# Kernel optimization log

Hardware: AMD Instinct MI355X
Metric: run time of the kernel (lower is better)

The kernel has to match this reference:

```python
import jax, jax.numpy as jnp
import numpy as np

D = 256; H = 8; HD = D // H; NK = 32; NLAYERS = 4; FF = 4 * D
B = 8; M = 768; N = 128; LT = 64; T = M + N + LT
SCALE = 1.0 / float(np.sqrt(HD))


def layer_norm(x, s, b):
    mu = x.mean(-1, keepdims=True)
    var = ((x - mu) ** 2).mean(-1, keepdims=True)
    return (x - mu) * jax.lax.rsqrt(var + 1e-5) * s + b


def sine_embed(pos, d):
    # MTR gen_sineembed_for_position: half dims for y, half for x, interleaved sin/cos
    half = d // 2
    dim_t = jnp.power(10000.0, 2.0 * (jnp.arange(half) // 2).astype(jnp.float32) / half)
    scale = 2.0 * np.pi
    def inter(e):
        return jnp.stack([jnp.sin(e[:, 0::2]), jnp.cos(e[:, 1::2])], -1).reshape(e.shape[0], -1)
    ex = pos[:, 0:1] * scale / dim_t
    ey = pos[:, 1:2] * scale / dim_t
    return jnp.concatenate([inter(ey), inter(ex)], -1)


def setup_inputs() -> dict:
    key = jax.random.key(0)
    ks = jax.random.split(key, 24)
    s = 0.02
    inp = {
        'map_token': jax.random.normal(ks[0], (B, M, D), jnp.float32),
        'agent_token': jax.random.normal(ks[1], (B, N, D), jnp.float32),
        'light_token': jax.random.normal(ks[2], (B, LT, D), jnp.float32),
        'map_position': jax.random.uniform(ks[3], (B, M, 2), jnp.float32) * 100.0,
        'agent_position': jax.random.uniform(ks[4], (B, N, 2), jnp.float32) * 100.0,
        'light_position': jax.random.uniform(ks[5], (B, LT, 2), jnp.float32) * 100.0,
        'map_valid_mask': jnp.ones((B, M), bool),
        'agent_valid_mask': jnp.ones((B, N), bool),
        'light_valid_mask': jnp.ones((B, LT), bool),
        'Wq': jax.random.normal(ks[6], (NLAYERS, D, D), jnp.float32) * s,
        'bq': jnp.zeros((NLAYERS, D), jnp.float32),
        'Wk': jax.random.normal(ks[7], (NLAYERS, D, D), jnp.float32) * s,
        'bk': jnp.zeros((NLAYERS, D), jnp.float32),
        'Wv': jax.random.normal(ks[8], (NLAYERS, D, D), jnp.float32) * s,
        'bv': jnp.zeros((NLAYERS, D), jnp.float32),
        'Wo': jax.random.normal(ks[9], (NLAYERS, D, D), jnp.float32) * s,
        'bo': jnp.zeros((NLAYERS, D), jnp.float32),
        'W1': jax.random.normal(ks[10], (NLAYERS, D, FF), jnp.float32) * s,
        'b1': jnp.zeros((NLAYERS, FF), jnp.float32),
        'W2': jax.random.normal(ks[11], (NLAYERS, FF, D), jnp.float32) * s,
        'b2': jnp.zeros((NLAYERS, D), jnp.float32),
        'ln1_s': jnp.ones((NLAYERS, D), jnp.float32),
        'ln1_b': jnp.zeros((NLAYERS, D), jnp.float32),
        'ln2_s': jnp.ones((NLAYERS, D), jnp.float32),
        'ln2_b': jnp.zeros((NLAYERS, D), jnp.float32),
    }
    return inp


def reference(map_token, agent_token, light_token, map_position, agent_position, light_position,
              map_valid_mask, agent_valid_mask, light_valid_mask,
              Wq, bq, Wk, bk, Wv, bv, Wo, bo, W1, b1, W2, b2, ln1_s, ln1_b, ln2_s, ln2_b):
    x = jnp.concatenate([map_token, agent_token, light_token], 1)             # [B,T,D]
    pos = jnp.concatenate([map_position, agent_position, light_position], 1)[..., :2]  # [B,T,2]
    # all tokens valid -> masked compaction is a static reshape
    xs = x.reshape(B * T, D)
    ps = pos.reshape(B * T, 2)
    # KNN within each scene (includes self, like knn_batch_mlogk on same set)
    d2 = jnp.sum((pos[:, :, None, :] - pos[:, None, :, :]) ** 2, -1)          # [B,T,T]
    _, idx = jax.lax.top_k(-d2, NK)                                            # [B,T,NK] local indices
    idx = (idx + (jnp.arange(B) * T)[:, None, None]).reshape(B * T, NK)        # global flat indices
    pe = sine_embed(ps, D)                                                     # [B*T,D]
    out = xs
    for l in range(NLAYERS):
        qk = out + pe
        q = (qk @ Wq[l] + bq[l]).reshape(-1, H, HD)
        k = (qk @ Wk[l] + bk[l]).reshape(-1, H, HD)
        v = (out @ Wv[l] + bv[l]).reshape(-1, H, HD)
        kn = k[idx]                                                            # [BT,NK,H,HD] gather
        vn = v[idx]
        att = jax.nn.softmax(jnp.einsum('nhd,nkhd->nhk', q, kn) * SCALE, axis=-1)
        a = jnp.einsum('nhk,nkhd->nhd', att, vn).reshape(-1, D) @ Wo[l] + bo[l]
        out = layer_norm(out + a, ln1_s[l], ln1_b[l])
        ff = jax.nn.relu(out @ W1[l] + b1[l]) @ W2[l] + b2[l]
        out = layer_norm(out + ff, ln2_s[l], ln2_b[l])
    full = out.reshape(B, T, D)
    return full[:, :M], full[:, M:M + N], full[:, M + N:]
```

## Files before the change

### kernel.cpp

```cpp
#include <hip/hip_runtime.h>
#include <math.h>

#define BB 8
#define MTOK 768
#define NTOK 128
#define LTOK 64
#define TT 960
#define BT 7680
#define DD 256
#define HH 8
#define HD 32
#define KNN 32
#define FFD 1024
#define NLAYERS 4
#define SCALE_ATT 0.17677669529663687f

typedef __attribute__((ext_vector_type(8))) short bfrag_t;
typedef __attribute__((ext_vector_type(4))) float accfrag_t;

__device__ __forceinline__ float b2f(unsigned short u) {
  union { unsigned int i; float f; } c; c.i = ((unsigned int)u) << 16; return c.f;
}
__device__ __forceinline__ unsigned short f2b(float f) {
  union { float f; unsigned int i; } c; c.f = f;
  return (unsigned short)((c.i + 0x7fffu + ((c.i >> 16) & 1u)) >> 16);
}
__device__ __forceinline__ float load_elem(const void* p, size_t i, int f) {
  return f ? b2f(((const unsigned short*)p)[i]) : ((const float*)p)[i];
}
__device__ __forceinline__ size_t pk_addr(int row, int col, int nks) {
  return ((size_t)((row >> 4) * nks + (col >> 5)) << 9)
       + (size_t)(((((col >> 3) & 3) << 4) + (row & 15)) * 8 + (col & 7));
}
__device__ __forceinline__ uint4 pack8(const float* v) {
  uint4 u;
  u.x = (unsigned)f2b(v[0]) | ((unsigned)f2b(v[1]) << 16);
  u.y = (unsigned)f2b(v[2]) | ((unsigned)f2b(v[3]) << 16);
  u.z = (unsigned)f2b(v[4]) | ((unsigned)f2b(v[5]) << 16);
  u.w = (unsigned)f2b(v[6]) | ((unsigned)f2b(v[7]) << 16);
  return u;
}
__device__ __forceinline__ int swiz_tok(int blk) { return (blk & 7) * TT + (blk >> 3); }

__global__ __launch_bounds__(256)
void detect_kernel(const void* tok, int* flag) {
  __shared__ int cnt;
  if (threadIdx.x == 0) cnt = 0;
  __syncthreads();
  const unsigned short* u = (const unsigned short*)tok;
  int ok = 0;
  for (int i = threadIdx.x; i < 1024; i += 256) {
    int e = (u[i] >> 7) & 0xFF;
    if (e >= 100 && e <= 140) ok++;
  }
  atomicAdd(&cnt, ok);
  __syncthreads();
  if (threadIdx.x == 0) *flag = (cnt >= 922) ? 1 : 0;
}

#define FB_BQ 0
#define FB_BK 1024
#define FB_BV 2048
#define FB_BO 3072
#define FB_B1 4096
#define FB_B2 8192
#define FB_LN1S 9216
#define FB_LN1B 10240
#define FB_LN2S 11264
#define FB_LN2B 12288
#define FB_TOTAL 13312
struct ParamSrc { const void* p[13]; };
__global__ __launch_bounds__(256)
void conv_misc_kernel(ParamSrc ps, const int* flag, float* __restrict__ dst,
                      float* __restrict__ posf) {
  int f = *flag;
  if (blockIdx.x < BB) {
    int b = blockIdx.x;
    for (int t = threadIdx.x; t < TT * 2; t += 256) {
      int tok = t >> 1, c = t & 1;
      const void* p; size_t idx;
      if (tok < MTOK)             { p = ps.p[10]; idx = (size_t)(b * MTOK + tok) * 2 + c; }
      else if (tok < MTOK + NTOK) { p = ps.p[11]; idx = (size_t)(b * NTOK + tok - MTOK) * 2 + c; }
      else                        { p = ps.p[12]; idx = (size_t)(b * LTOK + tok - MTOK - NTOK) * 2 + c; }
      posf[((size_t)b * TT + tok) * 2 + c] = load_elem(p, idx, f);
    }
    return;
  }
  int i = (blockIdx.x - BB) * 256 + threadIdx.x;
  if (i >= FB_TOTAL) return;
  int src; size_t off;
  if (i < 4096)      { src = i >> 10;              off = i & 1023; }
  else if (i < 8192) { src = 4;                    off = i - 4096; }
  else               { src = 5 + ((i - 8192) >> 10); off = (i - 8192) & 1023; }
  dst[i] = load_elem(ps.p[src], off, f);
}

struct PackSrc { const void* s[6]; };
__global__ __launch_bounds__(256)
void packW_kernel(PackSrc w, const int* flag,
                  unsigned short* __restrict__ Wqkvpk, unsigned short* __restrict__ Wopk,
                  unsigned short* __restrict__ W1pk, unsigned short* __restrict__ W2pk) {
  int f = *flag;
  int id = blockIdx.x * 256 + threadIdx.x;
  const void* src; unsigned short* dst; int layer, e, K, N;
  if (id < 786432) {
    layer = id / 196608; int rest = id % 196608; int sel = rest / 65536; e = rest % 65536;
    src = w.s[sel]; dst = Wqkvpk + id; K = 256; N = 256;
  } else if (id < 1048576) {
    int off = id - 786432; layer = off / 65536; e = off % 65536;
    src = w.s[3]; dst = Wopk + off; K = 256; N = 256;
  } else if (id < 2097152) {
    int off = id - 1048576; layer = off / 262144; e = off % 262144;
    src = w.s[4]; dst = W1pk + off; K = 256; N = 1024;
  } else {
    int off = id - 2097152; layer = off / 262144; e = off % 262144;
    src = w.s[5]; dst = W2pk + off; K = 1024; N = 256;
  }
  int nks = K >> 5;
  int cb = e / (nks * 512);
  int ks = (e / 512) % nks;
  int lane = (e >> 3) & 63, j = e & 7;
  int col = cb * 16 + (lane & 15);
  int k = ks * 32 + (lane >> 4) * 8 + j;
  size_t si = (size_t)layer * K * N + (size_t)k * N + col;
  *dst = f ? ((const unsigned short*)src)[si] : f2b(((const float*)src)[si]);
}

__global__ __launch_bounds__(256)
void prep_kernel(const void* mt, const void* at, const void* lt,
                 const float* __restrict__ posf, const int* flag,
                 unsigned short* __restrict__ pe_b, float* __restrict__ out_f,
                 unsigned short* __restrict__ pk1, unsigned short* __restrict__ qkpk) {
  int n = swiz_tok(blockIdx.x), d = threadIdx.x;
  int b = n / TT, t = n - b * TT;
  int f = *flag;
  const void* src; size_t si;
  if (t < MTOK)              { src = mt; si = (size_t)(b * MTOK + t) * DD + d; }
  else if (t < MTOK + NTOK)  { src = at; si = (size_t)(b * NTOK + (t - MTOK)) * DD + d; }
  else                       { src = lt; si = (size_t)(b * LTOK + (t - MTOK - NTOK)) * DD + d; }
  float x = load_elem(src, si, f);
  float px = posf[((size_t)b * TT + t) * 2 + 0];
  float py = posf[((size_t)b * TT + t) * 2 + 1];
  float coord = (d < 128) ? py : px;
  int j = d & 127;
  float expo = (float)(2 * (j >> 1)) / 128.0f;
  float dim_t = powf(10000.0f, expo);
  float e = coord * 6.283185307179586f / dim_t;
  float p = (j & 1) ? cosf(e) : sinf(e);
  size_t o = (size_t)n * DD + d;
  pe_b[o] = f2b(p);
  out_f[o] = x;
  size_t pa = pk_addr(n, d, 8);
  pk1[pa] = f2b(x);
  qkpk[pa] = f2b(x + p);
}

__device__ __forceinline__ unsigned long long shfl_xor_u64(unsigned long long v, int m) {
  unsigned lo = (unsigned)v, hi = (unsigned)(v >> 32);
  lo = (unsigned)__shfl_xor((int)lo, m);
  hi = (unsigned)__shfl_xor((int)hi, m);
  return ((unsigned long long)hi << 32) | (unsigned long long)lo;
}
__device__ __forceinline__ unsigned long long shfl_u64(unsigned long long v, int srcLane) {
  unsigned lo = (unsigned)v, hi = (unsigned)(v >> 32);
  lo = (unsigned)__shfl((int)lo, srcLane);
  hi = (unsigned)__shfl((int)hi, srcLane);
  return ((unsigned long long)hi << 32) | (unsigned long long)lo;
}
__device__ __forceinline__ unsigned long long bitonic64(unsigned long long key, int lane) {
#pragma unroll
  for (int kk = 2; kk <= 64; kk <<= 1) {
#pragma unroll
    for (int j = kk >> 1; j > 0; j >>= 1) {
      unsigned long long other = shfl_xor_u64(key, j);
      bool small_ = (lane & j) == 0;
      bool dir = (lane & kk) == 0;
      bool keep = ((key < other) == (small_ == dir));
      key = keep ? key : other;
    }
  }
  return key;
}

__global__ __launch_bounds__(256)
void knn_kernel(const float* __restrict__ posf, int* __restrict__ idx_out) {
  __shared__ float sx[TT], sy[TT];
  __shared__ unsigned long long cbuf[4][64];
  int b = blockIdx.x & 7;
  int qbase = (blockIdx.x >> 3) * 4;
  for (int t = threadIdx.x; t < TT; t += 256) {
    sx[t] = posf[((size_t)b * TT + t) * 2 + 0];
    sy[t] = posf[((size_t)b * TT + t) * 2 + 1];
  }
  __syncthreads();
  int wave = threadIdx.x >> 6, lane = threadIdx.x & 63;
  int t = qbase + wave;
  float qx = sx[t], qy = sy[t];

  unsigned long long k[15];
#pragma unroll
  for (int c = 0; c < 15; c++) {
    int j = c * 64 + lane;
    float dx = qx - sx[j], dy = qy - sy[j];
    float d2 = __fadd_rn(__fmul_rn(dx, dx), __fmul_rn(dy, dy));
    k[c] = ((unsigned long long)__float_as_uint(d2) << 32) | (unsigned)j;
  }

  unsigned long long lm = k[0];
#pragma unroll
  for (int c = 1; c < 15; c++) lm = (k[c] < lm) ? k[c] : lm;

  unsigned long long sm = bitonic64(lm, lane);
  unsigned long long thr = shfl_u64(sm, 31);

  int c_l = 0;
#pragma unroll
  for (int c = 0; c < 15; c++) c_l += (k[c] <= thr) ? 1 : 0;
  int inc = c_l;
#pragma unroll
  for (int o = 1; o < 64; o <<= 1) {
    int tt = __shfl_up(inc, o);
    inc += (lane >= o) ? tt : 0;
  }
  int total = __shfl(inc, 63);
  int pos = inc - c_l;

  if (total <= 64) {
    unsigned long long* wb = cbuf[wave];
#pragma unroll
    for (int c = 0; c < 15; c++) {
      if (k[c] <= thr) { wb[pos] = k[c]; pos++; }
    }
    unsigned long long cand = (lane < total) ? wb[lane] : ~0ull;
    cand = bitonic64(cand, lane);
    if (lane < KNN)
      idx_out[((size_t)(b * TT + t)) * KNN + lane] = b * TT + (int)(cand & 0xFFFFFFFFu);
  } else {
    unsigned res = 0;
    for (int i = 0; i < KNN; i++) {
      unsigned long long m = k[0];
#pragma unroll
      for (int c = 1; c < 15; c++) m = (k[c] < m) ? k[c] : m;
#pragma unroll
      for (int o = 32; o > 0; o >>= 1) {
        unsigned long long om = shfl_xor_u64(m, o);
        m = (om < m) ? om : m;
      }
      if (lane == i) res = (unsigned)(m & 0xFFFFFFFFu);
      int owner = (int)(m & 63u), ch = (int)(((unsigned)(m & 0xFFFFFFFFu)) >> 6);
      if (lane == owner) {
#pragma unroll
        for (int c = 0; c < 15; c++) if (c == ch) k[c] = ~0ull;
      }
    }
    if (lane < KNN)
      idx_out[((size_t)(b * TT + t)) * KNN + lane] = b * TT + (int)res;
  }
}

template<int NKS>
__device__ __forceinline__ void wavegemm(const unsigned short* __restrict__ Apk,
                                         const unsigned short* __restrict__ Bpk,
                                         int rb, int cb0, accfrag_t (&acc)[4]) {
  const int lane = threadIdx.x & 63;
  accfrag_t z = {0.f, 0.f, 0.f, 0.f};
#pragma unroll
  for (int nt = 0; nt < 4; nt++) acc[nt] = z;
  const unsigned short* ap = Apk + ((size_t)rb * NKS * 512 + lane * 8);
  const unsigned short* bp = Bpk + ((size_t)cb0 * NKS * 512 + lane * 8);
#pragma unroll 4
  for (int ks = 0; ks < NKS; ks++) {
    bfrag_t a = *(const bfrag_t*)(ap + ks * 512);
#pragma unroll
    for (int nt = 0; nt < 4; nt++) {
      bfrag_t b = *(const bfrag_t*)(bp + (size_t)(nt * NKS + ks) * 512);
      acc[nt] = __builtin_amdgcn_mfma_f32_16x16x32_bf16(a, b, acc[nt], 0, 0, 0);
    }
  }
}

__global__ __launch_bounds__(256)
void qkv_kernel(const unsigned short* __restrict__ qkpk,
                const unsigned short* __restrict__ outpk,
                const unsigned short* __restrict__ Wl,
                const float* __restrict__ pb, int l,
                unsigned short* __restrict__ QKV) {
  int scene = blockIdx.x & 7, r = blockIdx.x >> 3;
  int rbg = r % 15, cgall = r / 15;
  int wave = threadIdx.x >> 6, lane = threadIdx.x & 63;
  int rb = scene * 60 + rbg * 4 + wave;
  int sel = cgall >> 2, cg = cgall & 3;
  const unsigned short* A = (sel < 2) ? qkpk : outpk;
  const unsigned short* B = Wl + sel * 65536;
  const float* bias = pb + sel * 1024 + l * 256;
  accfrag_t acc[4];
  wavegemm<8>(A, B, rb, cg * 4, acc);
  int l16 = lane & 15, lq = lane >> 4;
  unsigned short* C = QKV + (size_t)sel * BT * DD;
#pragma unroll
  for (int nt = 0; nt < 4; nt++) {
    int col = cg * 64 + nt * 16 + l16;
    float bv = bias[col];
#pragma unroll
    for (int r4 = 0; r4 < 4; r4++) {
      int row = rb * 16 + lq * 4 + r4;
      C[(size_t)row * DD + col] = f2b(acc[nt][r4] + bv);
    }
  }
}

__global__ __launch_bounds__(256)
void attn_kernel(const unsigned short* __restrict__ QKV,
                 const int* __restrict__ idx,
                 unsigned short* __restrict__ attnpk) {
  __shared__ unsigned short kn[KNN][DD + 8];
  __shared__ unsigned short vn[KNN][DD + 8];
  __shared__ float qs[DD];
  __shared__ float att[HH][KNN];
  __shared__ int nb[KNN];
  const unsigned short* Q = QKV;
  const unsigned short* K = QKV + (size_t)BT * DD;
  const unsigned short* V = QKV + 2 * (size_t)BT * DD;
  int n = swiz_tok(blockIdx.x), tid = threadIdx.x;
  if (tid < KNN) nb[tid] = idx[n * KNN + tid];
  qs[tid] = b2f(Q[(size_t)n * DD + tid]);
  __syncthreads();
#pragma unroll
  for (int p = 0; p < 4; p++) {
    int e = p * 256 + tid;
    int r = e >> 5, c8 = (e & 31) * 8;
    int srow = nb[r];
    *(uint4*)(&kn[r][c8]) = *(const uint4*)(K + (size_t)srow * DD + c8);
    *(uint4*)(&vn[r][c8]) = *(const uint4*)(V + (size_t)srow * DD + c8);
  }
  __syncthreads();
  int h = tid >> 5, kk = tid & 31;
  float dot = 0.0f;
#pragma unroll
  for (int d = 0; d < HD; d++) dot += qs[h * HD + d] * b2f(kn[kk][h * HD + d]);
  float sc = dot * SCALE_ATT;
  float mx = sc;
#pragma unroll
  for (int o = 16; o > 0; o >>= 1) mx = fmaxf(mx, __shfl_xor(mx, o, 32));
  float ex = expf(sc - mx);
  float sm = ex;
#pragma unroll
  for (int o = 16; o > 0; o >>= 1) sm += __shfl_xor(sm, o, 32);
  att[h][kk] = ex / sm;
  __syncthreads();
  int d = kk;
  float oacc = 0.0f;
#pragma unroll
  for (int k2 = 0; k2 < KNN; k2++) oacc += att[h][k2] * b2f(vn[k2][h * HD + d]);
  attnpk[pk_addr(n, tid, 8)] = f2b(oacc);
}

__global__ __launch_bounds__(256)
void wo_ln1_kernel(const unsigned short* __restrict__ attnpk,
                   const unsigned short* __restrict__ Wl,
                   const float* __restrict__ bo,
                   float* __restrict__ yf,
                   unsigned short* __restrict__ xpk,
                   const float* __restrict__ g, const float* __restrict__ bta) {
  __shared__ float ps1[4][16], ps2[4][16];
  int scene = blockIdx.x & 7, rbs = blockIdx.x >> 3;
  int wave = threadIdx.x >> 6, lane = threadIdx.x & 63;
  int rb = scene * 60 + rbs;
  accfrag_t acc[4];
  wavegemm<8>(attnpk, Wl, rb, wave * 4, acc);
  int l16 = lane & 15, lq = lane >> 4;
  float val[4][4];
  float s[4] = {0.f, 0.f, 0.f, 0.f}, s2[4] = {0.f, 0.f, 0.f, 0.f};
#pragma unroll
  for (int nt = 0; nt < 4; nt++) {
    int col = wave * 64 + nt * 16 + l16;
    float bv = bo[col];
#pragma unroll
    for (int r4 = 0; r4 < 4; r4++) {
      int row = rb * 16 + lq * 4 + r4;
      float x = acc[nt][r4] + bv + yf[(size_t)row * DD + col];
      val[nt][r4] = x; s[r4] += x; s2[r4] += x * x;
    }
  }
#pragma unroll
  for (int o = 1; o < 16; o <<= 1) {
#pragma unroll
    for (int r4 = 0; r4 < 4; r4++) { s[r4] += __shfl_xor(s[r4], o); s2[r4] += __shfl_xor(s2[r4], o); }
  }
  if (l16 == 0) {
#pragma unroll
    for (int r4 = 0; r4 < 4; r4++) { ps1[wave][lq * 4 + r4] = s[r4]; ps2[wave][lq * 4 + r4] = s2[r4]; }
  }
  __syncthreads();
  float mu[4], rstd[4];
#pragma unroll
  for (int r4 = 0; r4 < 4; r4++) {
    int r16 = lq * 4 + r4;
    float ts  = ps1[0][r16] + ps1[1][r16] + ps1[2][r16] + ps1[3][r16];
    float ts2 = ps2[0][r16] + ps2[1][r16] + ps2[2][r16] + ps2[3][r16];
    mu[r4] = ts * (1.0f / 256.0f);
    float var = ts2 * (1.0f / 256.0f) - mu[r4] * mu[r4];
    rstd[r4] = 1.0f / sqrtf(fmaxf(var, 0.f) + 1e-5f);
  }
#pragma unroll
  for (int nt = 0; nt < 4; nt++) {
    int col = wave * 64 + nt * 16 + l16;
    float gg = g[col], bb = bta[col];
#pragma unroll
    for (int r4 = 0; r4 < 4; r4++) {
      int row = rb * 16 + lq * 4 + r4;
      float y = (val[nt][r4] - mu[r4]) * rstd[r4] * gg + bb;
      yf[(size_t)row * DD + col] = y;
      xpk[pk_addr(row, col, 8)] = f2b(y);
    }
  }
}

__global__ __launch_bounds__(256)
void ffn1_kernel(const unsigned short* __restrict__ xpk,
                 const unsigned short* __restrict__ Wl,
                 const float* __restrict__ b1,
                 unsigned short* __restrict__ hpk) {
  int scene = blockIdx.x & 7, r = blockIdx.x >> 3;
  int rbg = r % 15, cg = r / 15;
  int wave = threadIdx.x >> 6, lane = threadIdx.x & 63;
  int rb = scene * 60 + rbg * 4 + wave;
  accfrag_t acc[4];
  wavegemm<8>(xpk, Wl, rb, cg * 4, acc);
  int l16 = lane & 15, lq = lane >> 4;
#pragma unroll
  for (int nt = 0; nt < 4; nt++) {
    int col = cg * 64 + nt * 16 + l16;
    float bv = b1[col];
#pragma unroll
    for (int r4 = 0; r4 < 4; r4++) {
      int row = rb * 16 + lq * 4 + r4;
      hpk[pk_addr(row, col, 32)] = f2b(fmaxf(acc[nt][r4] + bv, 0.0f));
    }
  }
}

template<bool LAST>
__global__ __launch_bounds__(256)
void ffn2_ln2_kernel(const unsigned short* __restrict__ hpk,
                     const unsigned short* __restrict__ Wl,
                     const float* __restrict__ b2,
                     float* __restrict__ yf,
                     unsigned short* __restrict__ outpk, unsigned short* __restrict__ qkpk,
                     const unsigned short* __restrict__ pe_b,
                     const float* __restrict__ g, const float* __restrict__ bta,
                     void* __restrict__ dout, const int* __restrict__ flag) {
  __shared__ float ps1[4][16], ps2[4][16];
  int scene = blockIdx.x & 7, rbs = blockIdx.x >> 3;
  int wave = threadIdx.x >> 6, lane = threadIdx.x & 63;
  int rb = scene * 60 + rbs;
  accfrag_t acc[4];
  wavegemm<32>(hpk, Wl, rb, wave * 4, acc);
  int l16 = lane & 15, lq = lane >> 4;
  float val[4][4];
  float s[4] = {0.f, 0.f, 0.f, 0.f}, s2[4] = {0.f, 0.f, 0.f, 0.f};
#pragma unroll
  for (int nt = 0; nt < 4; nt++) {
    int col = wave * 64 + nt * 16 + l16;
    float bv = b2[col];
#pragma unroll
    for (int r4 = 0; r4 < 4; r4++) {
      int row = rb * 16 + lq * 4 + r4;
      float x = acc[nt][r4] + bv + yf[(size_t)row * DD + col];
      val[nt][r4] = x; s[r4] += x; s2[r4] += x * x;
    }
  }
#pragma unroll
  for (int o = 1; o < 16; o <<= 1) {
#pragma unroll
    for (int r4 = 0; r4 < 4; r4++) { s[r4] += __shfl_xor(s[r4], o); s2[r4] += __shfl_xor(s2[r4], o); }
  }
  if (l16 == 0) {
#pragma unroll
    for (int r4 = 0; r4 < 4; r4++) { ps1[wave][lq * 4 + r4] = s[r4]; ps2[wave][lq * 4 + r4] = s2[r4]; }
  }
  __syncthreads();
  float mu[4], rstd[4];
#pragma unroll
  for (int r4 = 0; r4 < 4; r4++) {
    int r16 = lq * 4 + r4;
    float ts  = ps1[0][r16] + ps1[1][r16] + ps1[2][r16] + ps1[3][r16];
    float ts2 = ps2[0][r16] + ps2[1][r16] + ps2[2][r16] + ps2[3][r16];
    mu[r4] = ts * (1.0f / 256.0f);
    float var = ts2 * (1.0f / 256.0f) - mu[r4] * mu[r4];
    rstd[r4] = 1.0f / sqrtf(fmaxf(var, 0.f) + 1e-5f);
  }
  int fl = LAST ? *flag : 0;
#pragma unroll
  for (int nt = 0; nt < 4; nt++) {
    int col = wave * 64 + nt * 16 + l16;
    float gg = g[col], bb = bta[col];
#pragma unroll
    for (int r4 = 0; r4 < 4; r4++) {
      int row = rb * 16 + lq * 4 + r4;
      float y = (val[nt][r4] - mu[r4]) * rstd[r4] * gg + bb;
      if (!LAST) {
        yf[(size_t)row * DD + col] = y;
        outpk[pk_addr(row, col, 8)] = f2b(y);
        float q = y + b2f(pe_b[(size_t)row * DD + col]);
        qkpk[pk_addr(row, col, 8)] = f2b(q);
      } else {
        int t = rbs * 16 + lq * 4 + r4;
        size_t o;
        if (t < MTOK)             o = (size_t)(scene * MTOK + t) * DD + col;
        else if (t < MTOK + NTOK) o = (size_t)BB * MTOK * DD + (size_t)(scene * NTOK + (t - MTOK)) * DD + col;
        else                      o = (size_t)BB * MTOK * DD + (size_t)BB * NTOK * DD
                                    + (size_t)(scene * LTOK + (t - MTOK - NTOK)) * DD + col;
        if (fl) ((unsigned short*)dout)[o] = f2b(y);
        else    ((float*)dout)[o] = y;
      }
    }
  }
}

extern "C" void kernel_launch(void* const* d_in, const int* in_sizes, int n_in,
                              void* d_out, int out_size, void* d_ws, size_t ws_size,
                              hipStream_t stream) {
  const void* map_tok   = d_in[0];
  const void* agent_tok = d_in[1];
  const void* light_tok = d_in[2];
  const void* map_pos   = d_in[3];
  const void* agent_pos = d_in[4];
  const void* light_pos = d_in[5];
  const void* Wq  = d_in[9];
  const void* bq  = d_in[10];
  const void* Wk  = d_in[11];
  const void* bk  = d_in[12];
  const void* Wv  = d_in[13];
  const void* bv  = d_in[14];
  const void* Wo  = d_in[15];
  const void* bo  = d_in[16];
  const void* W1  = d_in[17];
  const void* b1  = d_in[18];
  const void* W2  = d_in[19];
  const void* b2  = d_in[20];
  const void* ln1s = d_in[21];
  const void* ln1b = d_in[22];
  const void* ln2s = d_in[23];
  const void* ln2b = d_in[24];

  size_t off = 0;
  char* base = (char*)d_ws;
  auto take = [&](size_t bytes) { char* p = base + off; off += (bytes + 255) & ~(size_t)255; return (void*)p; };
  int*   flag  = (int*)take(256);
  float* posf  = (float*)take((size_t)BT * 2 * 4);
  float* pbuf  = (float*)take((size_t)FB_TOTAL * 4);
  unsigned short* pe_b = (unsigned short*)take((size_t)BT * DD * 2);
  float* out_f = (float*)take((size_t)BT * DD * 4);
  unsigned short* pk1  = (unsigned short*)take((size_t)BT * DD * 2);
  unsigned short* qkpk = (unsigned short*)take((size_t)BT * DD * 2);
  unsigned short* QKV  = (unsigned short*)take((size_t)3 * BT * DD * 2);
  unsigned short* attnpk = (unsigned short*)take((size_t)BT * DD * 2);
  unsigned short* hpk  = (unsigned short*)take((size_t)BT * FFD * 2);
  int* idxb = (int*)take((size_t)BT * KNN * 4);
  unsigned short* Wqkvpk = (unsigned short*)take((size_t)NLAYERS * 3 * DD * DD * 2);
  unsigned short* Wopk   = (unsigned short*)take((size_t)NLAYERS * DD * DD * 2);
  unsigned short* W1pk   = (unsigned short*)take((size_t)NLAYERS * DD * FFD * 2);
  unsigned short* W2pk   = (unsigned short*)take((size_t)NLAYERS * DD * FFD * 2);

  detect_kernel<<<1, 256, 0, stream>>>(map_tok, flag);
  ParamSrc ps; ps.p[0]=bq; ps.p[1]=bk; ps.p[2]=bv; ps.p[3]=bo; ps.p[4]=b1;
  ps.p[5]=b2; ps.p[6]=ln1s; ps.p[7]=ln1b; ps.p[8]=ln2s; ps.p[9]=ln2b;
  ps.p[10]=map_pos; ps.p[11]=agent_pos; ps.p[12]=light_pos;
  conv_misc_kernel<<<BB + (FB_TOTAL + 255) / 256, 256, 0, stream>>>(ps, flag, pbuf, posf);

  PackSrc pw; pw.s[0]=Wq; pw.s[1]=Wk; pw.s[2]=Wv; pw.s[3]=Wo; pw.s[4]=W1; pw.s[5]=W2;
  packW_kernel<<<12288, 256, 0, stream>>>(pw, flag, Wqkvpk, Wopk, W1pk, W2pk);

  prep_kernel<<<BT, 256, 0, stream>>>(map_tok, agent_tok, light_tok, posf, flag,
                                      pe_b, out_f, pk1, qkpk);
  knn_kernel<<<1920, 256, 0, stream>>>(posf, idxb);

  for (int l = 0; l < NLAYERS; l++) {
    qkv_kernel<<<1440, 256, 0, stream>>>(qkpk, pk1, Wqkvpk + (size_t)l * 3 * 65536,
                                         pbuf, l, QKV);
    attn_kernel<<<BT, 256, 0, stream>>>(QKV, idxb, attnpk);
    wo_ln1_kernel<<<480, 256, 0, stream>>>(attnpk, Wopk + (size_t)l * 65536,
                                           pbuf + FB_BO + l * 256, out_f, pk1,
                                           pbuf + FB_LN1S + l * 256, pbuf + FB_LN1B + l * 256);
    ffn1_kernel<<<1920, 256, 0, stream>>>(pk1, W1pk + (size_t)l * 262144,
                                          pbuf + FB_B1 + l * 1024, hpk);
    if (l < NLAYERS - 1)
      ffn2_ln2_kernel<false><<<480, 256, 0, stream>>>(hpk, W2pk + (size_t)l * 262144,
                                                      pbuf + FB_B2 + l * 256, out_f, pk1, qkpk, pe_b,
                                                      pbuf + FB_LN2S + l * 256, pbuf + FB_LN2B + l * 256,
                                                      d_out, flag);
    else
      ffn2_ln2_kernel<true><<<480, 256, 0, stream>>>(hpk, W2pk + (size_t)l * 262144,
                                                     pbuf + FB_B2 + l * 256, out_f, pk1, qkpk, pe_b,
                                                     pbuf + FB_LN2S + l * 256, pbuf + FB_LN2B + l * 256,
                                                     d_out, flag);
  }
}
```

Baseline: 473.2 us.

## Fuse Wo+LN1, FFN1 and FFN2+LN2 into a single per-row-block kernel

Merges the three post-attention kernels into one kernel per 16-row block. The LN1 output and the ReLU hidden activations stay in shared memory instead of going through the global hpk buffer, and the residual is kept in registers. This removes two launches per layer and the global round-trip of the 1024-wide hidden tensor. In exchange, FFN1 drops from 1920 blocks to 480, each block uses about 40KB of LDS which limits occupancy, and every block rereads the full W1 and W2 matrices.

```diff
diff --git a/kernel.cpp b/kernel.cpp
--- a/kernel.cpp
+++ b/kernel.cpp
@@ -31,14 +31,6 @@
 __device__ __forceinline__ size_t pk_addr(int row, int col, int nks) {
   return ((size_t)((row >> 4) * nks + (col >> 5)) << 9)
        + (size_t)(((((col >> 3) & 3) << 4) + (row & 15)) * 8 + (col & 7));
-}
-__device__ __forceinline__ uint4 pack8(const float* v) {
-  uint4 u;
-  u.x = (unsigned)f2b(v[0]) | ((unsigned)f2b(v[1]) << 16);
-  u.y = (unsigned)f2b(v[2]) | ((unsigned)f2b(v[3]) << 16);
-  u.z = (unsigned)f2b(v[4]) | ((unsigned)f2b(v[5]) << 16);
-  u.w = (unsigned)f2b(v[6]) | ((unsigned)f2b(v[7]) << 16);
-  return u;
 }
 __device__ __forceinline__ int swiz_tok(int blk) { return (blk & 7) * TT + (blk >> 3); }
 
@@ -205,7 +197,6 @@
     float d2 = __fadd_rn(__fmul_rn(dx, dx), __fmul_rn(dy, dy));
     k[c] = ((unsigned long long)__float_as_uint(d2) << 32) | (unsigned)j;
   }
-
   unsigned long long lm = k[0];
 #pragma unroll
   for (int c = 1; c < 15; c++) lm = (k[c] < lm) ? k[c] : lm;
@@ -355,21 +346,32 @@
   attnpk[pk_addr(n, tid, 8)] = f2b(oacc);
 }
 
-__global__ __launch_bounds__(256)
-void wo_ln1_kernel(const unsigned short* __restrict__ attnpk,
-                   const unsigned short* __restrict__ Wl,
-                   const float* __restrict__ bo,
-                   float* __restrict__ yf,
-                   unsigned short* __restrict__ xpk,
-                   const float* __restrict__ g, const float* __restrict__ bta) {
+template<bool LAST>
+__global__ __launch_bounds__(256)
+void ffn_block_kernel(const unsigned short* __restrict__ attnpk,
+                      const unsigned short* __restrict__ Wo,
+                      const unsigned short* __restrict__ W1,
+                      const unsigned short* __restrict__ W2,
+                      const float* __restrict__ bo,
+                      const float* __restrict__ b1,
+                      const float* __restrict__ b2,
+                      float* __restrict__ yf,
+                      unsigned short* __restrict__ outpk, unsigned short* __restrict__ qkpk,
+                      const unsigned short* __restrict__ pe_b,
+                      const float* __restrict__ g1, const float* __restrict__ t1,
+                      const float* __restrict__ g2, const float* __restrict__ t2,
+                      void* __restrict__ dout, const int* __restrict__ flag) {
+  __shared__ unsigned short xls[8 * 512];
+  __shared__ unsigned short hls[32 * 512];
   __shared__ float ps1[4][16], ps2[4][16];
   int scene = blockIdx.x & 7, rbs = blockIdx.x >> 3;
   int wave = threadIdx.x >> 6, lane = threadIdx.x & 63;
   int rb = scene * 60 + rbs;
+  int l16 = lane & 15, lq = lane >> 4;
+
   accfrag_t acc[4];
-  wavegemm<8>(attnpk, Wl, rb, wave * 4, acc);
-  int l16 = lane & 15, lq = lane >> 4;
-  float val[4][4];
+  wavegemm<8>(attnpk, Wo, rb, wave * 4, acc);
+  float y[4][4];
   float s[4] = {0.f, 0.f, 0.f, 0.f}, s2[4] = {0.f, 0.f, 0.f, 0.f};
 #pragma unroll
   for (int nt = 0; nt < 4; nt++) {
@@ -379,7 +381,7 @@
     for (int r4 = 0; r4 < 4; r4++) {
       int row = rb * 16 + lq * 4 + r4;
       float x = acc[nt][r4] + bv + yf[(size_t)row * DD + col];
-      val[nt][r4] = x; s[r4] += x; s2[r4] += x * x;
+      y[nt][r4] = x; s[r4] += x; s2[r4] += x * x;
     }
   }
 #pragma unroll
@@ -392,127 +394,92 @@
     for (int r4 = 0; r4 < 4; r4++) { ps1[wave][lq * 4 + r4] = s[r4]; ps2[wave][lq * 4 + r4] = s2[r4]; }
   }
   __syncthreads();
-  float mu[4], rstd[4];
 #pragma unroll
   for (int r4 = 0; r4 < 4; r4++) {
     int r16 = lq * 4 + r4;
     float ts  = ps1[0][r16] + ps1[1][r16] + ps1[2][r16] + ps1[3][r16];
     float ts2 = ps2[0][r16] + ps2[1][r16] + ps2[2][r16] + ps2[3][r16];
-    mu[r4] = ts * (1.0f / 256.0f);
-    float var = ts2 * (1.0f / 256.0f) - mu[r4] * mu[r4];
-    rstd[r4] = 1.0f / sqrtf(fmaxf(var, 0.f) + 1e-5f);
-  }
-#pragma unroll
-  for (int nt = 0; nt < 4; nt++) {
-    int col = wave * 64 + nt * 16 + l16;
-    float gg = g[col], bb = bta[col];
-#pragma unroll
-    for (int r4 = 0; r4 < 4; r4++) {
-      int row = rb * 16 + lq * 4 + r4;
-      float y = (val[nt][r4] - mu[r4]) * rstd[r4] * gg + bb;
-      yf[(size_t)row * DD + col] = y;
-      xpk[pk_addr(row, col, 8)] = f2b(y);
-    }
-  }
-}
-
-__global__ __launch_bounds__(256)
-void ffn1_kernel(const unsigned short* __restrict__ xpk,
-                 const unsigned short* __restrict__ Wl,
-                 const float* __restrict__ b1,
-                 unsigned short* __restrict__ hpk) {
-  int scene = blockIdx.x & 7, r = blockIdx.x >> 3;
-  int rbg = r % 15, cg = r / 15;
-  int wave = threadIdx.x >> 6, lane = threadIdx.x & 63;
-  int rb = scene * 60 + rbg * 4 + wave;
-  accfrag_t acc[4];
-  wavegemm<8>(xpk, Wl, rb, cg * 4, acc);
-  int l16 = lane & 15, lq = lane >> 4;
-#pragma unroll
-  for (int nt = 0; nt < 4; nt++) {
-    int col = cg * 64 + nt * 16 + l16;
-    float bv = b1[col];
-#pragma unroll
-    for (int r4 = 0; r4 < 4; r4++) {
-      int row = rb * 16 + lq * 4 + r4;
-      hpk[pk_addr(row, col, 32)] = f2b(fmaxf(acc[nt][r4] + bv, 0.0f));
-    }
-  }
-}
-
-template<bool LAST>
-__global__ __launch_bounds__(256)
-void ffn2_ln2_kernel(const unsigned short* __restrict__ hpk,
-                     const unsigned short* __restrict__ Wl,
-                     const float* __restrict__ b2,
-                     float* __restrict__ yf,
-                     unsigned short* __restrict__ outpk, unsigned short* __restrict__ qkpk,
-                     const unsigned short* __restrict__ pe_b,
-                     const float* __restrict__ g, const float* __restrict__ bta,
-                     void* __restrict__ dout, const int* __restrict__ flag) {
-  __shared__ float ps1[4][16], ps2[4][16];
-  int scene = blockIdx.x & 7, rbs = blockIdx.x >> 3;
-  int wave = threadIdx.x >> 6, lane = threadIdx.x & 63;
-  int rb = scene * 60 + rbs;
-  accfrag_t acc[4];
-  wavegemm<32>(hpk, Wl, rb, wave * 4, acc);
-  int l16 = lane & 15, lq = lane >> 4;
-  float val[4][4];
-  float s[4] = {0.f, 0.f, 0.f, 0.f}, s2[4] = {0.f, 0.f, 0.f, 0.f};
+    float mu = ts * (1.0f / 256.0f);
+    float var = ts2 * (1.0f / 256.0f) - mu * mu;
+    float rstd = 1.0f / sqrtf(fmaxf(var, 0.f) + 1e-5f);
+#pragma unroll
+    for (int nt = 0; nt < 4; nt++) {
+      int col = wave * 64 + nt * 16 + l16;
+      float v = (y[nt][r4] - mu) * rstd * g1[col] + t1[col];
+      y[nt][r4] = v;
+      xls[pk_addr(r16, col, 8)] = f2b(v);
+    }
+  }
+  __syncthreads();
+
+#pragma unroll
+  for (int i = 0; i < 4; i++) {
+    int cg = wave * 4 + i;
+    accfrag_t a2[4];
+    wavegemm<8>(xls, W1, 0, cg * 4, a2);
+#pragma unroll
+    for (int nt = 0; nt < 4; nt++) {
+      int col = cg * 64 + nt * 16 + l16;
+      float bv = b1[col];
+#pragma unroll
+      for (int r4 = 0; r4 < 4; r4++)
+        hls[pk_addr(lq * 4 + r4, col, 32)] = f2b(fmaxf(a2[nt][r4] + bv, 0.0f));
+    }
+  }
+  __syncthreads();
+
+  accfrag_t a3[4];
+  wavegemm<32>(hls, W2, 0, wave * 4, a3);
+  float v2[4][4];
+  float s3[4] = {0.f, 0.f, 0.f, 0.f}, s4[4] = {0.f, 0.f, 0.f, 0.f};
 #pragma unroll
   for (int nt = 0; nt < 4; nt++) {
     int col = wave * 64 + nt * 16 + l16;
     float bv = b2[col];
 #pragma unroll
     for (int r4 = 0; r4 < 4; r4++) {
-      int row = rb * 16 + lq * 4 + r4;
-      float x = acc[nt][r4] + bv + yf[(size_t)row * DD + col];
-      val[nt][r4] = x; s[r4] += x; s2[r4] += x * x;
+      float x = a3[nt][r4] + bv + y[nt][r4];
+      v2[nt][r4] = x; s3[r4] += x; s4[r4] += x * x;
     }
   }
 #pragma unroll
   for (int o = 1; o < 16; o <<= 1) {
 #pragma unroll
-    for (int r4 = 0; r4 < 4; r4++) { s[r4] += __shfl_xor(s[r4], o); s2[r4] += __shfl_xor(s2[r4], o); }
+    for (int r4 = 0; r4 < 4; r4++) { s3[r4] += __shfl_xor(s3[r4], o); s4[r4] += __shfl_xor(s4[r4], o); }
   }
   if (l16 == 0) {
 #pragma unroll
-    for (int r4 = 0; r4 < 4; r4++) { ps1[wave][lq * 4 + r4] = s[r4]; ps2[wave][lq * 4 + r4] = s2[r4]; }
-  }
-  __syncthreads();
-  float mu[4], rstd[4];
+    for (int r4 = 0; r4 < 4; r4++) { ps1[wave][lq * 4 + r4] = s3[r4]; ps2[wave][lq * 4 + r4] = s4[r4]; }
+  }
+  __syncthreads();
+  int fl = LAST ? *flag : 0;
 #pragma unroll
   for (int r4 = 0; r4 < 4; r4++) {
     int r16 = lq * 4 + r4;
     float ts  = ps1[0][r16] + ps1[1][r16] + ps1[2][r16] + ps1[3][r16];
     float ts2 = ps2[0][r16] + ps2[1][r16] + ps2[2][r16] + ps2[3][r16];
-    mu[r4] = ts * (1.0f / 256.0f);
-    float var = ts2 * (1.0f / 256.0f) - mu[r4] * mu[r4];
-    rstd[r4] = 1.0f / sqrtf(fmaxf(var, 0.f) + 1e-5f);
-  }
-  int fl = LAST ? *flag : 0;
-#pragma unroll
-  for (int nt = 0; nt < 4; nt++) {
-    int col = wave * 64 + nt * 16 + l16;
-    float gg = g[col], bb = bta[col];
-#pragma unroll
-    for (int r4 = 0; r4 < 4; r4++) {
-      int row = rb * 16 + lq * 4 + r4;
-      float y = (val[nt][r4] - mu[r4]) * rstd[r4] * gg + bb;
+    float mu = ts * (1.0f / 256.0f);
+    float var = ts2 * (1.0f / 256.0f) - mu * mu;
+    float rstd = 1.0f / sqrtf(fmaxf(var, 0.f) + 1e-5f);
+#pragma unroll
+    for (int nt = 0; nt < 4; nt++) {
+      int col = wave * 64 + nt * 16 + l16;
+      float yv = (v2[nt][r4] - mu) * rstd * g2[col] + t2[col];
+      int row = rb * 16 + r16;
       if (!LAST) {
-        yf[(size_t)row * DD + col] = y;
-        outpk[pk_addr(row, col, 8)] = f2b(y);
-        float q = y + b2f(pe_b[(size_t)row * DD + col]);
+        yf[(size_t)row * DD + col] = yv;
+        outpk[pk_addr(row, col, 8)] = f2b(yv);
+        float q = yv + b2f(pe_b[(size_t)row * DD + col]);
         qkpk[pk_addr(row, col, 8)] = f2b(q);
       } else {
-        int t = rbs * 16 + lq * 4 + r4;
+        int t = rbs * 16 + r16;
         size_t o;
         if (t < MTOK)             o = (size_t)(scene * MTOK + t) * DD + col;
         else if (t < MTOK + NTOK) o = (size_t)BB * MTOK * DD + (size_t)(scene * NTOK + (t - MTOK)) * DD + col;
         else                      o = (size_t)BB * MTOK * DD + (size_t)BB * NTOK * DD
                                     + (size_t)(scene * LTOK + (t - MTOK - NTOK)) * DD + col;
-        if (fl) ((unsigned short*)dout)[o] = f2b(y);
-        else    ((float*)dout)[o] = y;
+        if (fl) ((unsigned short*)dout)[o] = f2b(yv);
+        else    ((float*)dout)[o] = yv;
       }
     }
   }
@@ -556,7 +523,6 @@
   unsigned short* qkpk = (unsigned short*)take((size_t)BT * DD * 2);
   unsigned short* QKV  = (unsigned short*)take((size_t)3 * BT * DD * 2);
   unsigned short* attnpk = (unsigned short*)take((size_t)BT * DD * 2);
-  unsigned short* hpk  = (unsigned short*)take((size_t)BT * FFD * 2);
   int* idxb = (int*)take((size_t)BT * KNN * 4);
   unsigned short* Wqkvpk = (unsigned short*)take((size_t)NLAYERS * 3 * DD * DD * 2);
   unsigned short* Wopk   = (unsigned short*)take((size_t)NLAYERS * DD * DD * 2);
@@ -580,20 +546,21 @@
     qkv_kernel<<<1440, 256, 0, stream>>>(qkpk, pk1, Wqkvpk + (size_t)l * 3 * 65536,
                                          pbuf, l, QKV);
     attn_kernel<<<BT, 256, 0, stream>>>(QKV, idxb, attnpk);
-    wo_ln1_kernel<<<480, 256, 0, stream>>>(attnpk, Wopk + (size_t)l * 65536,
-                                           pbuf + FB_BO + l * 256, out_f, pk1,
-                                           pbuf + FB_LN1S + l * 256, pbuf + FB_LN1B + l * 256);
-    ffn1_kernel<<<1920, 256, 0, stream>>>(pk1, W1pk + (size_t)l * 262144,
-                                          pbuf + FB_B1 + l * 1024, hpk);
     if (l < NLAYERS - 1)
-      ffn2_ln2_kernel<false><<<480, 256, 0, stream>>>(hpk, W2pk + (size_t)l * 262144,
-                                                      pbuf + FB_B2 + l * 256, out_f, pk1, qkpk, pe_b,
-                                                      pbuf + FB_LN2S + l * 256, pbuf + FB_LN2B + l * 256,
-                                                      d_out, flag);
+      ffn_block_kernel<false><<<480, 256, 0, stream>>>(
+          attnpk, Wopk + (size_t)l * 65536, W1pk + (size_t)l * 262144, W2pk + (size_t)l * 262144,
+          pbuf + FB_BO + l * 256, pbuf + FB_B1 + l * 1024, pbuf + FB_B2 + l * 256,
+          out_f, pk1, qkpk, pe_b,
+          pbuf + FB_LN1S + l * 256, pbuf + FB_LN1B + l * 256,
+          pbuf + FB_LN2S + l * 256, pbuf + FB_LN2B + l * 256,
+          d_out, flag);
     else
-      ffn2_ln2_kernel<true><<<480, 256, 0, stream>>>(hpk, W2pk + (size_t)l * 262144,
-                                                     pbuf + FB_B2 + l * 256, out_f, pk1, qkpk, pe_b,
-                                                     pbuf + FB_LN2S + l * 256, pbuf + FB_LN2B + l * 256,
-                                                     d_out, flag);
-  }
-}
+      ffn_block_kernel<true><<<480, 256, 0, stream>>>(
+          attnpk, Wopk + (size_t)l * 65536, W1pk + (size_t)l * 262144, W2pk + (size_t)l * 262144,
+          pbuf + FB_BO + l * 256, pbuf + FB_B1 + l * 1024, pbuf + FB_B2 + l * 256,
+          out_f, pk1, qkpk, pe_b,
+          pbuf + FB_LN1S + l * 256, pbuf + FB_LN1B + l * 256,
+          pbuf + FB_LN2S + l * 256, pbuf + FB_LN2B + l * 256,
+          d_out, flag);
+  }
+}
```

Result: faster. 429.9 us (-9.2%).
